# Kernel optimization log

Hardware: AMD Instinct MI355X
Metric: run time of the kernel (lower is better)

## Reference

```python
import jax, jax.numpy as jnp
import numpy as np

EPS = 1e-8  # torch.nn.CosineSimilarity default eps


def setup_inputs() -> dict:
    key = jax.random.key(0)
    k1, k2 = jax.random.split(key)
    N, C, K = 131072, 128, 512
    embeddings = jax.random.normal(k1, (N, C), dtype=jnp.float32)
    prototypes = jax.random.normal(k2, (K, C), dtype=jnp.float32)
    return {"embeddings": embeddings, "prototypes": prototypes}


def reference(embeddings, prototypes):
    # Cosine similarity between each embedding and each prototype, expressed as
    # a normalized GEMM instead of the O(N*K*C) broadcast the torch code builds.
    e = embeddings / jnp.maximum(
        jnp.linalg.norm(embeddings, axis=-1, keepdims=True), EPS)
    p = prototypes / jnp.maximum(
        jnp.linalg.norm(prototypes, axis=-1, keepdims=True), EPS)
    cos = jnp.einsum('nc,kc->nk', e, p)  # (N, K)
    dists = 1.0 - cos
    scores = -(dists * dists)
    return scores
```

## Files before the change

### kernel.cpp

```cpp
#include <hip/hip_runtime.h>

#define EPS_F 1e-8f

typedef float  f32x4  __attribute__((ext_vector_type(4)));
typedef __bf16 bf16x8 __attribute__((ext_vector_type(8)));
typedef unsigned short u16x4 __attribute__((ext_vector_type(4)));
typedef unsigned short u16x8 __attribute__((ext_vector_type(8)));

__device__ inline unsigned short f2bf(float x) {
  unsigned int u = __float_as_uint(x);
  u += 0x7fffu + ((u >> 16) & 1u);
  return (unsigned short)(u >> 16);
}

__global__ __launch_bounds__(256) void proto_norm_kernel(
    const float* __restrict__ proto, unsigned short* __restrict__ Bn)
{
  const int tid = threadIdx.x;
  const int g   = tid & 31;
  const int row = blockIdx.x * 8 + (tid >> 5);
  const float4 v = *(const float4*)&proto[row * 128 + g * 4];
  float ss = v.x*v.x + v.y*v.y + v.z*v.z + v.w*v.w;
  #pragma unroll
  for (int m = 16; m >= 1; m >>= 1) ss += __shfl_xor(ss, m);
  const float rn = 1.0f / fmaxf(sqrtf(ss), EPS_F);
  u16x4 b;
  b[0] = f2bf(v.x * rn); b[1] = f2bf(v.y * rn);
  b[2] = f2bf(v.z * rn); b[3] = f2bf(v.w * rn);
  *(u16x4*)&Bn[row * 128 + g * 4] = b;
}

__global__ __launch_bounds__(256, 3) void hproto_kernel(
    const float* __restrict__ emb, const unsigned short* __restrict__ Bn,
    float* __restrict__ out)
{
  constexpr int CD = 128;
  constexpr int KP = 512;

  const int tid  = threadIdx.x;
  const int lane = tid & 63;
  const int wave = tid >> 6;
  const int lo   = lane & 15;
  const int hi   = lane >> 4;
  const long rbase = (long)blockIdx.x * 128 + wave * 32;

  bf16x8 bufA[2][4], bufB[2][4];
  auto loadB = [&](bf16x8 (&dst)[2][4], int s) {
    const unsigned short* bp = Bn + (s * 32 + lo) * CD + hi * 8;
    #pragma unroll
    for (int n = 0; n < 2; ++n)
      #pragma unroll
      for (int kk = 0; kk < 4; ++kk)
        dst[n][kk] = *(const bf16x8*)(bp + n * 16 * CD + kk * 32);
  };

  loadB(bufA, 0);

  bf16x8 af[2][4];
  float  re[2];
  #pragma unroll
  for (int m = 0; m < 2; ++m) {
    const float* rp = emb + (rbase + m * 16 + lo) * CD + hi * 8;
    f32x4 a[4][2];
    #pragma unroll
    for (int kk = 0; kk < 4; ++kk) {
      a[kk][0] = *(const f32x4*)(rp + kk * 32);
      a[kk][1] = *(const f32x4*)(rp + kk * 32 + 4);
    }
    float ss = 0.f;
    #pragma unroll
    for (int kk = 0; kk < 4; ++kk) {
      u16x8 b;
      #pragma unroll
      for (int j = 0; j < 4; ++j) {
        ss += a[kk][0][j] * a[kk][0][j] + a[kk][1][j] * a[kk][1][j];
        b[j]     = f2bf(a[kk][0][j]);
        b[4 + j] = f2bf(a[kk][1][j]);
      }
      af[m][kk] = __builtin_bit_cast(bf16x8, b);
    }
    ss += __shfl_xor(ss, 16);
    ss += __shfl_xor(ss, 32);
    re[m] = 1.0f / fmaxf(sqrtf(ss), EPS_F);
  }

  float* const ob = out + (rbase + lo) * KP + hi * 4;

  auto compute = [&](bf16x8 (&buf)[2][4], int s) {
    f32x4 acc[2][2];
    #pragma unroll
    for (int m = 0; m < 2; ++m)
      #pragma unroll
      for (int n = 0; n < 2; ++n) acc[m][n] = f32x4{0.f, 0.f, 0.f, 0.f};
    #pragma unroll
    for (int kk = 0; kk < 4; ++kk)
      #pragma unroll
      for (int m = 0; m < 2; ++m)
        #pragma unroll
        for (int n = 0; n < 2; ++n)
          acc[m][n] = __builtin_amdgcn_mfma_f32_16x16x32_bf16(
              buf[n][kk], af[m][kk], acc[m][n], 0, 0, 0);
    #pragma unroll
    for (int m = 0; m < 2; ++m)
      #pragma unroll
      for (int n = 0; n < 2; ++n) {
        f32x4 v;
        #pragma unroll
        for (int j = 0; j < 4; ++j) {
          float d = 1.0f - acc[m][n][j] * re[m];
          v[j] = -(d * d);
        }
        __builtin_nontemporal_store(v, (f32x4*)(ob + m * 16 * KP + s * 32 + n * 16));
      }
  };

  #pragma unroll 1
  for (int t = 0; t < 8; ++t) {
    const int s0 = t * 2;
    loadB(bufB, s0 + 1);
    compute(bufA, s0);
    if (t < 7) loadB(bufA, s0 + 2);
    compute(bufB, s0 + 1);
  }
}

extern "C" void kernel_launch(void* const* d_in, const int* in_sizes, int n_in,
                              void* d_out, int out_size, void* d_ws, size_t ws_size,
                              hipStream_t stream) {
  const float* emb   = (const float*)d_in[0];
  const float* proto = (const float*)d_in[1];
  float* out = (float*)d_out;
  unsigned short* Bn = (unsigned short*)d_ws;
  const int C = 128;
  const int N = in_sizes[0] / C;
  const int K = in_sizes[1] / C;
  proto_norm_kernel<<<K / 8, 256, 0, stream>>>(proto, Bn);
  hproto_kernel<<<N / 128, 256, 0, stream>>>(emb, Bn, out);
}
```

Measured before the change: 353.5 us.

## Shrink prototype stage to 16 columns and raise occupancy to four blocks

```diff
diff --git a/kernel.cpp b/kernel.cpp
--- a/kernel.cpp
+++ b/kernel.cpp
@@ -30,7 +30,7 @@
   *(u16x4*)&Bn[row * 128 + g * 4] = b;
 }
 
-__global__ __launch_bounds__(256, 3) void hproto_kernel(
+__global__ __launch_bounds__(256, 4) void hproto_kernel(
     const float* __restrict__ emb, const unsigned short* __restrict__ Bn,
     float* __restrict__ out)
 {
@@ -44,29 +44,36 @@
   const int hi   = lane >> 4;
   const long rbase = (long)blockIdx.x * 128 + wave * 32;
 
-  bf16x8 bufA[2][4], bufB[2][4];
-  auto loadB = [&](bf16x8 (&dst)[2][4], int s) {
-    const unsigned short* bp = Bn + (s * 32 + lo) * CD + hi * 8;
+  bf16x8 af[2][4];
+  float  re[2];
+  bf16x8 bufA[4], bufB[4];
+
+  auto loadB = [&](bf16x8 (&dst)[4], int s) {
+    const unsigned short* bp = Bn + (s * 16 + lo) * CD + hi * 8;
     #pragma unroll
-    for (int n = 0; n < 2; ++n)
-      #pragma unroll
-      for (int kk = 0; kk < 4; ++kk)
-        dst[n][kk] = *(const bf16x8*)(bp + n * 16 * CD + kk * 32);
+    for (int kk = 0; kk < 4; ++kk)
+      dst[kk] = *(const bf16x8*)(bp + kk * 32);
   };
 
-  loadB(bufA, 0);
-
-  bf16x8 af[2][4];
-  float  re[2];
-  #pragma unroll
-  for (int m = 0; m < 2; ++m) {
-    const float* rp = emb + (rbase + m * 16 + lo) * CD + hi * 8;
-    f32x4 a[4][2];
+  f32x4 a0[4][2], a1[4][2];
+  {
+    const float* rp0 = emb + (rbase + lo) * CD + hi * 8;
+    const float* rp1 = emb + (rbase + 16 + lo) * CD + hi * 8;
     #pragma unroll
     for (int kk = 0; kk < 4; ++kk) {
-      a[kk][0] = *(const f32x4*)(rp + kk * 32);
-      a[kk][1] = *(const f32x4*)(rp + kk * 32 + 4);
+      a0[kk][0] = *(const f32x4*)(rp0 + kk * 32);
+      a0[kk][1] = *(const f32x4*)(rp0 + kk * 32 + 4);
     }
+    loadB(bufA, 0);
+    loadB(bufB, 1);
+    #pragma unroll
+    for (int kk = 0; kk < 4; ++kk) {
+      a1[kk][0] = *(const f32x4*)(rp1 + kk * 32);
+      a1[kk][1] = *(const f32x4*)(rp1 + kk * 32 + 4);
+    }
+  }
+
+  auto convert = [&](f32x4 (&a)[4][2], int m) {
     float ss = 0.f;
     #pragma unroll
     for (int kk = 0; kk < 4; ++kk) {
@@ -82,45 +89,37 @@
     ss += __shfl_xor(ss, 16);
     ss += __shfl_xor(ss, 32);
     re[m] = 1.0f / fmaxf(sqrtf(ss), EPS_F);
-  }
+  };
+  convert(a0, 0);
+  convert(a1, 1);
 
   float* const ob = out + (rbase + lo) * KP + hi * 4;
 
-  auto compute = [&](bf16x8 (&buf)[2][4], int s) {
-    f32x4 acc[2][2];
+  auto compute = [&](bf16x8 (&buf)[4], int s) {
+    f32x4 acc[2] = {f32x4{0.f,0.f,0.f,0.f}, f32x4{0.f,0.f,0.f,0.f}};
     #pragma unroll
-    for (int m = 0; m < 2; ++m)
+    for (int kk = 0; kk < 4; ++kk) {
+      acc[0] = __builtin_amdgcn_mfma_f32_16x16x32_bf16(buf[kk], af[0][kk], acc[0], 0, 0, 0);
+      acc[1] = __builtin_amdgcn_mfma_f32_16x16x32_bf16(buf[kk], af[1][kk], acc[1], 0, 0, 0);
+    }
+    #pragma unroll
+    for (int m = 0; m < 2; ++m) {
+      f32x4 v;
       #pragma unroll
-      for (int n = 0; n < 2; ++n) acc[m][n] = f32x4{0.f, 0.f, 0.f, 0.f};
-    #pragma unroll
-    for (int kk = 0; kk < 4; ++kk)
-      #pragma unroll
-      for (int m = 0; m < 2; ++m)
-        #pragma unroll
-        for (int n = 0; n < 2; ++n)
-          acc[m][n] = __builtin_amdgcn_mfma_f32_16x16x32_bf16(
-              buf[n][kk], af[m][kk], acc[m][n], 0, 0, 0);
-    #pragma unroll
-    for (int m = 0; m < 2; ++m)
-      #pragma unroll
-      for (int n = 0; n < 2; ++n) {
-        f32x4 v;
-        #pragma unroll
-        for (int j = 0; j < 4; ++j) {
-          float d = 1.0f - acc[m][n][j] * re[m];
-          v[j] = -(d * d);
-        }
-        __builtin_nontemporal_store(v, (f32x4*)(ob + m * 16 * KP + s * 32 + n * 16));
+      for (int j = 0; j < 4; ++j) {
+        float d = fmaf(-acc[m][j], re[m], 1.0f);
+        v[j] = -(d * d);
       }
+      __builtin_nontemporal_store(v, (f32x4*)(ob + m * 16 * KP + s * 16));
+    }
   };
 
   #pragma unroll 1
-  for (int t = 0; t < 8; ++t) {
-    const int s0 = t * 2;
-    loadB(bufB, s0 + 1);
-    compute(bufA, s0);
-    if (t < 7) loadB(bufA, s0 + 2);
-    compute(bufB, s0 + 1);
+  for (int t = 0; t < 16; ++t) {
+    compute(bufA, 2 * t);
+    if (t < 15) loadB(bufA, 2 * t + 2);
+    compute(bufB, 2 * t + 1);
+    if (t < 15) loadB(bufB, 2 * t + 3);
   }
 }
 
```

Measured after the change: 359.1 us. Within noise of the previous version (+1.6%).
